# Kernel optimization log

Hardware: AMD Instinct MI355X
Metric: run time of the kernel (lower is better)

The kernel has to match this reference:

```python
import jax, jax.numpy as jnp
import numpy as np

MAX_DEG = 10
MIN_DEG = 0
N_FEAT = 128
NB_FILTER = 128
BATCH = 128
DEG_COUNT = 30000                      # atoms per degree bucket (static)
N_ATOMS = (MAX_DEG + 1) * DEG_COUNT    # 330000, atoms sorted by degree (deg0 first)
NB_AFFINE = 3 * MAX_DEG + (2 - MIN_DEG)  # 32
EPS = 1e-5


def setup_inputs() -> dict:
    key = jax.random.key(0)
    ks = jax.random.split(key, 16)
    atoms = jax.random.normal(ks[0], (N_ATOMS, N_FEAT), dtype=jnp.float32)
    membership = jax.random.randint(ks[1], (N_ATOMS,), 0, BATCH)
    # deg_slice[d] = [start, count] for degree d (atoms sorted by degree)
    deg_slice = jnp.stack([jnp.arange(MAX_DEG + 1) * DEG_COUNT,
                           jnp.full((MAX_DEG + 1,), DEG_COUNT)], axis=1)
    inp = {"atoms": atoms, "deg_slice": deg_slice, "membership": membership}
    for d in range(1, MAX_DEG + 1):
        inp[f"adj{d}"] = jax.random.randint(ks[1 + d], (DEG_COUNT, d), 0, N_ATOMS)
    glorot = (2.0 / (N_FEAT + NB_FILTER)) ** 0.5
    inp["W"] = jax.random.normal(ks[12], (NB_AFFINE, N_FEAT, NB_FILTER), dtype=jnp.float32) * glorot
    inp["b"] = jnp.zeros((NB_AFFINE, NB_FILTER), dtype=jnp.float32)
    inp["gamma"] = jnp.ones((NB_FILTER,), dtype=jnp.float32)
    inp["beta"] = jnp.zeros((NB_FILTER,), dtype=jnp.float32)
    return inp


def _self_slice(atoms, deg):
    return jax.lax.dynamic_slice_in_dim(atoms, deg * DEG_COUNT, DEG_COUNT, axis=0)


def _norm(x, gamma, beta):
    m = jnp.mean(x, axis=-1, keepdims=True)
    std = jnp.sqrt(jnp.var(x, axis=-1, keepdims=True) + EPS)
    return gamma * ((x - m) / (std + EPS)) + beta


def _forward(atoms, W, b, gamma, beta, membership, adjs):
    # W consumption order matches the TF iterator: for deg=1..max_deg -> (rel, self),
    # then deg0 self at index 2*MAX_DEG, then gather affines deg1..max_deg, deg0 last.
    rel_outs = [None] * (MAX_DEG + 1)
    gather_outs = [None] * (MAX_DEG + 1)
    for d in range(1, MAX_DEG + 1):
        neigh = jnp.sum(atoms[adjs[d - 1]], axis=1)          # (COUNT, F) gather+sum
        self_a = _self_slice(atoms, d)                        # (COUNT, F)
        i_rel, i_self = 2 * (d - 1), 2 * d - 1
        rel_outs[d] = (neigh @ W[i_rel] + b[i_rel]) + (self_a @ W[i_self] + b[i_self])
        i_g = 2 * MAX_DEG + d
        gather_outs[d] = self_a @ W[i_g] + b[i_g]
    self0 = _self_slice(atoms, 0)
    rel_outs[0] = self0 @ W[2 * MAX_DEG] + b[2 * MAX_DEG]
    gather_outs[0] = self0 @ W[NB_AFFINE - 1] + b[NB_AFFINE - 1]

    activated = jnp.concatenate(rel_outs, axis=0)             # (N_ATOMS, NB_FILTER)
    gathered = jnp.concatenate(gather_outs, axis=0)           # (N_ATOMS, NB_FILTER)
    # graph_gather: per-molecule sum (dynamic_partition + reduce_sum)
    atom_gather = jax.ops.segment_sum(gathered, membership, num_segments=BATCH)

    xn = _norm(activated, gamma, beta)                        # per-row "BN" as in source
    yn = _norm(atom_gather, gamma, beta)
    # gather_node: per-molecule max of normalized atom features
    g = jax.ops.segment_max(xn, membership, num_segments=BATCH)
    return xn, yn, g


def reference(atoms, deg_slice, membership, adj1, adj2, adj3, adj4, adj5,
              adj6, adj7, adj8, adj9, adj10, W, b, gamma, beta):
    adjs = (adj1, adj2, adj3, adj4, adj5, adj6, adj7, adj8, adj9, adj10)
    return _forward(atoms, W, b, gamma, beta, membership, adjs)
```

## Files before the change

### kernel.cpp

```cpp
#include <hip/hip_runtime.h>
#include <stdint.h>

#define MAX_DEG   10
#define DEG_COUNT 30000
#define N_ATOMS   330000
#define NF        128
#define BATCH     128
#define SORT_BLOCKS 256

typedef __attribute__((ext_vector_type(8))) short bf16x8;
typedef __attribute__((ext_vector_type(4))) float f32x4;

__device__ __forceinline__ float bf2f(unsigned short h) {
  union { unsigned u; float f; } v; v.u = ((unsigned)h) << 16; return v.f;
}
__device__ __forceinline__ unsigned short f2bf(float f) {
  union { float f; unsigned u; } v; v.f = f;
  unsigned u = v.u;
  unsigned r = (u + 0x7fffu + ((u >> 16) & 1u)) >> 16;
  return (unsigned short)r;
}

struct AdjPtrs { const int* p[10]; };

#define NEG_INF_BITS 0xFF800000

__global__ __launch_bounds__(256) void k_cast(const float4* __restrict__ src,
                                              ushort4* __restrict__ dst) {
  size_t i = (size_t)blockIdx.x * 256 + threadIdx.x;
  float4 v = src[i];
  ushort4 o;
  o.x = f2bf(v.x); o.y = f2bf(v.y); o.z = f2bf(v.z); o.w = f2bf(v.w);
  dst[i] = o;
}

__global__ __launch_bounds__(256) void k_build_b(const float* __restrict__ W,
                                                 unsigned short* __restrict__ BcatT) {
  int idx = blockIdx.x * 256 + threadIdx.x;
  if (idx >= 11 * 256 * 256) return;
  int d = idx >> 16;
  int rem = idx & 65535;
  int n = rem >> 8;
  int k = rem & 255;
  float v = 0.f;
  if (k < 128) {
    if (n < 128 && d >= 1) v = W[(2 * (d - 1)) * 16384 + k * 128 + n];
  } else {
    int ks = k - 128;
    if (n < 128) { int wi = (d >= 1) ? (2 * d - 1) : 20; v = W[wi * 16384 + ks * 128 + n]; }
    else         { int wi = (d >= 1) ? (20 + d)   : 31; v = W[wi * 16384 + ks * 128 + (n - 128)]; }
  }
  BcatT[idx] = f2bf(v);
}

__global__ __launch_bounds__(256) void k_build_bias(const float* __restrict__ b,
                                                    float* __restrict__ biascat) {
  int idx = blockIdx.x * 256 + threadIdx.x;
  if (idx >= 11 * 256) return;
  int d = idx >> 8, n = idx & 255;
  float f;
  if (n < 128) {
    if (d >= 1) f = b[(2 * (d - 1)) * 128 + n] + b[(2 * d - 1) * 128 + n];
    else        f = b[20 * 128 + n];
  } else {
    int j = n - 128;
    f = (d >= 1) ? b[(20 + d) * 128 + j] : b[31 * 128 + j];
  }
  biascat[idx] = f;
}

template<int D>
__device__ __forceinline__ void nsum_body2(const unsigned* __restrict__ atomsU,
                                           const int* __restrict__ a,
                                           int lane,
                                           unsigned* __restrict__ out) {
  int myIdx = (lane < 2 * D) ? a[lane] : 0;
  unsigned xs[2 * D];
#pragma unroll
  for (int j = 0; j < 2 * D; ++j) {
    int nbr = __shfl(myIdx, j, 64);
    xs[j] = atomsU[(size_t)nbr * 64 + lane];
  }
  float s0a = 0.f, s1a = 0.f, s0b = 0.f, s1b = 0.f;
#pragma unroll
  for (int j = 0; j < D; ++j) {
    s0a += bf2f((unsigned short)(xs[j] & 0xffff));
    s1a += bf2f((unsigned short)(xs[j] >> 16));
  }
#pragma unroll
  for (int j = D; j < 2 * D; ++j) {
    s0b += bf2f((unsigned short)(xs[j] & 0xffff));
    s1b += bf2f((unsigned short)(xs[j] >> 16));
  }
  out[lane]      = (unsigned)f2bf(s0a) | ((unsigned)f2bf(s1a) << 16);
  out[64 + lane] = (unsigned)f2bf(s0b) | ((unsigned)f2bf(s1b) << 16);
}

__global__ __launch_bounds__(256) void k_nsum(const unsigned* __restrict__ atomsU,
                                              AdjPtrs adj,
                                              unsigned* __restrict__ nsumU) {
  int wave = threadIdx.x >> 6;
  int lane = threadIdx.x & 63;
  int row0 = blockIdx.x * 8 + wave * 2;
  int d = row0 / DEG_COUNT;
  unsigned* out = nsumU + (size_t)row0 * 64;
  if (d == 0) { out[lane] = 0u; out[64 + lane] = 0u; return; }
  int r = row0 - d * DEG_COUNT;
  const int* a = adj.p[d - 1] + (size_t)r * d;
  switch (d) {
    case 1:  nsum_body2<1>(atomsU, a, lane, out); break;
    case 2:  nsum_body2<2>(atomsU, a, lane, out); break;
    case 3:  nsum_body2<3>(atomsU, a, lane, out); break;
    case 4:  nsum_body2<4>(atomsU, a, lane, out); break;
    case 5:  nsum_body2<5>(atomsU, a, lane, out); break;
    case 6:  nsum_body2<6>(atomsU, a, lane, out); break;
    case 7:  nsum_body2<7>(atomsU, a, lane, out); break;
    case 8:  nsum_body2<8>(atomsU, a, lane, out); break;
    case 9:  nsum_body2<9>(atomsU, a, lane, out); break;
    default: nsum_body2<10>(atomsU, a, lane, out); break;
  }
}

__global__ __launch_bounds__(512, 2) void k_gemm(
    const unsigned short* __restrict__ atomsBf,
    const unsigned short* __restrict__ nsum,
    const unsigned short* __restrict__ BcatT,
    const float* __restrict__ biascat,
    const float* __restrict__ gamma,
    const float* __restrict__ beta,
    float* __restrict__ out0,
    unsigned short* __restrict__ gath)
{
  const int d = blockIdx.y;
  const int rowTile = blockIdx.x;
  const int tid = threadIdx.x;
  const int lane = tid & 63;
  const int wave = tid >> 6;
  const int m16 = lane & 15;
  const int g = lane >> 4;

  __shared__ unsigned short Bs[256 * 256];

  const unsigned short* Bd = BcatT + d * 65536;

#pragma unroll
  for (int it = 0; it < 16; ++it) {
    int flat = it * 512 + tid;
    int row = flat >> 5;
    int c = flat & 31;
    uint4 v = *(const uint4*)(Bd + row * 256 + c * 8);
    int kb = (c * 16) ^ ((row & 7) << 4);
    *(uint4*)((char*)Bs + row * 512 + kb) = v;
  }

  const int rowBase0 = rowTile * 256 + wave * 32;
  bf16x8 af0[8], af1[8];
  {
    int rbL = rowBase0 + m16; if (rbL > DEG_COUNT - 1) rbL = DEG_COUNT - 1;
    size_t gr = (size_t)d * DEG_COUNT + rbL;
#pragma unroll
    for (int ks = 0; ks < 4; ++ks)
      af0[ks] = *(const bf16x8*)(nsum + gr * 128 + ks * 32 + g * 8);
#pragma unroll
    for (int ks = 4; ks < 8; ++ks)
      af0[ks] = *(const bf16x8*)(atomsBf + gr * 128 + (ks - 4) * 32 + g * 8);
  }
  {
    int rbL = rowBase0 + 16 + m16; if (rbL > DEG_COUNT - 1) rbL = DEG_COUNT - 1;
    size_t gr = (size_t)d * DEG_COUNT + rbL;
#pragma unroll
    for (int ks = 0; ks < 4; ++ks)
      af1[ks] = *(const bf16x8*)(nsum + gr * 128 + ks * 32 + g * 8);
#pragma unroll
    for (int ks = 4; ks < 8; ++ks)
      af1[ks] = *(const bf16x8*)(atomsBf + gr * 128 + (ks - 4) * 32 + g * 8);
  }

  __syncthreads();

  const int ldsMask = (m16 & 7) << 4;

  f32x4 acc0[16], acc1[16];
#pragma unroll
  for (int ct = 0; ct < 16; ++ct) {
    acc0[ct] = (f32x4){0.f, 0.f, 0.f, 0.f};
    acc1[ct] = (f32x4){0.f, 0.f, 0.f, 0.f};
  }

#pragma unroll
  for (int ct = 0; ct < 16; ++ct) {
    const char* bbase = (const char*)Bs + (ct * 16 + m16) * 512;
    bf16x8 bf[8];
#pragma unroll
    for (int ks = 0; ks < 8; ++ks)
      bf[ks] = *(const bf16x8*)(bbase + ((ks * 64 + g * 16) ^ ldsMask));
#pragma unroll
    for (int ks = 0; ks < 8; ++ks) {
      acc0[ct] = __builtin_amdgcn_mfma_f32_16x16x32_bf16(af0[ks], bf[ks], acc0[ct], 0, 0, 0);
      acc1[ct] = __builtin_amdgcn_mfma_f32_16x16x32_bf16(af1[ks], bf[ks], acc1[ct], 0, 0, 0);
    }
  }

  float bias_[16], gam[8], bet[8];
#pragma unroll
  for (int ct = 0; ct < 16; ++ct) bias_[ct] = biascat[d * 256 + ct * 16 + m16];
#pragma unroll
  for (int ct = 0; ct < 8; ++ct) {
    gam[ct] = gamma[ct * 16 + m16];
    bet[ct] = beta[ct * 16 + m16];
  }

#pragma unroll
  for (int sub = 0; sub < 2; ++sub) {
    const int rowBase = rowBase0 + sub * 16;
    f32x4* acc = (sub == 0) ? acc0 : acc1;

#pragma unroll
    for (int ct = 0; ct < 16; ++ct)
#pragma unroll
      for (int r = 0; r < 4; ++r) acc[ct][r] += bias_[ct];

    float s[4], qq[4];
#pragma unroll
    for (int r = 0; r < 4; ++r) {
      s[r] = 0.f; qq[r] = 0.f;
#pragma unroll
      for (int ct = 0; ct < 8; ++ct) {
        float v = acc[ct][r];
        s[r] += v; qq[r] += v * v;
      }
    }
#pragma unroll
    for (int off = 8; off >= 1; off >>= 1) {
#pragma unroll
      for (int r = 0; r < 4; ++r) {
        s[r]  += __shfl_xor(s[r],  off, 64);
        qq[r] += __shfl_xor(qq[r], off, 64);
      }
    }

#pragma unroll
    for (int r = 0; r < 4; ++r) {
      int rb = rowBase + g * 4 + r;
      float mean = s[r] * (1.0f / 128.0f);
      float var  = qq[r] * (1.0f / 128.0f) - mean * mean;
      float inv  = 1.0f / (sqrtf(var + 1e-5f) + 1e-5f);
      if (rb < DEG_COUNT) {
        size_t grow = (size_t)d * DEG_COUNT + rb;
#pragma unroll
        for (int ct = 0; ct < 8; ++ct)
          out0[grow * 128 + ct * 16 + m16] = gam[ct] * ((acc[ct][r] - mean) * inv) + bet[ct];
#pragma unroll
        for (int ct = 8; ct < 16; ++ct)
          gath[grow * 128 + (ct - 8) * 16 + m16] = f2bf(acc[ct][r]);
      }
    }
  }
}

__global__ __launch_bounds__(256) void k_hist2(const int* __restrict__ membership,
                                               int* __restrict__ blockHist) {
  __shared__ int bins[BATCH];
  int tid = threadIdx.x;
  if (tid < BATCH) bins[tid] = 0;
  __syncthreads();
  const int chunk = (N_ATOMS + SORT_BLOCKS - 1) / SORT_BLOCKS;
  int lo = blockIdx.x * chunk, hi = min(lo + chunk, N_ATOMS);
  for (int i = lo + tid; i < hi; i += 256)
    atomicAdd(&bins[membership[i]], 1);
  __syncthreads();
  if (tid < BATCH) blockHist[blockIdx.x * BATCH + tid] = bins[tid];
}

__global__ __launch_bounds__(128) void k_scan2(const int* __restrict__ blockHist,
                                               int* __restrict__ off,
                                               int* __restrict__ base,
                                               int* __restrict__ hist) {
  int m = threadIdx.x;
  int tot = 0;
  for (int b = 0; b < SORT_BLOCKS; ++b) tot += blockHist[b * BATCH + m];
  hist[m] = tot;
  __shared__ int t[BATCH];
  t[m] = tot;
  __syncthreads();
  int acc = 0;
  for (int i = 0; i < m; ++i) acc += t[i];
  base[m] = acc;
  int run = acc;
  for (int b = 0; b < SORT_BLOCKS; ++b) {
    off[b * BATCH + m] = run;
    run += blockHist[b * BATCH + m];
  }
}

__global__ __launch_bounds__(256) void k_scatter2(const int* __restrict__ membership,
                                                  const int* __restrict__ off,
                                                  int* __restrict__ perm) {
  __shared__ int bins[BATCH];
  int tid = threadIdx.x;
  if (tid < BATCH) bins[tid] = off[blockIdx.x * BATCH + tid];
  __syncthreads();
  const int chunk = (N_ATOMS + SORT_BLOCKS - 1) / SORT_BLOCKS;
  int lo = blockIdx.x * chunk, hi = min(lo + chunk, N_ATOMS);
  for (int i = lo + tid; i < hi; i += 256) {
    int m = membership[i];
    int pos = atomicAdd(&bins[m], 1);
    perm[pos] = i;
  }
}

__global__ __launch_bounds__(512) void k_reduce(
    const float2* __restrict__ xnV,
    const unsigned* __restrict__ gathU,
    const int* __restrict__ perm,
    const int* __restrict__ base,
    const int* __restrict__ hist,
    float2* __restrict__ psum4,
    float2* __restrict__ pmax4)
{
  const int m = blockIdx.x >> 2;
  const int s = blockIdx.x & 3;
  const int b0 = base[m], cnt = hist[m];
  const int lo = b0 + (cnt * s) / 4;
  const int hi = b0 + (cnt * (s + 1)) / 4;
  const int wave = threadIdx.x >> 6, lane = threadIdx.x & 63;

  const float NEG_INF = __int_as_float((int)NEG_INF_BITS);
  float mx0 = NEG_INF, mx1 = NEG_INF, s0 = 0.f, s1 = 0.f;

#pragma unroll 4
  for (int i = lo + wave; i < hi; i += 8) {
    int r = perm[i];
    float2 x = xnV[(size_t)r * 64 + lane];
    unsigned gg = gathU[(size_t)r * 64 + lane];
    mx0 = fmaxf(mx0, x.x);
    mx1 = fmaxf(mx1, x.y);
    s0 += bf2f((unsigned short)(gg & 0xffff));
    s1 += bf2f((unsigned short)(gg >> 16));
  }

  __shared__ float2 sumT[8][64];
  __shared__ float2 maxT[8][64];
  sumT[wave][lane] = make_float2(s0, s1);
  maxT[wave][lane] = make_float2(mx0, mx1);
  __syncthreads();

  if (threadIdx.x < 64) {
    int l = threadIdx.x;
    float2 ss = sumT[0][l];
    float2 mm = maxT[0][l];
#pragma unroll
    for (int w = 1; w < 8; ++w) {
      float2 a = sumT[w][l]; ss.x += a.x; ss.y += a.y;
      float2 b = maxT[w][l]; mm.x = fmaxf(mm.x, b.x); mm.y = fmaxf(mm.y, b.y);
    }
    psum4[(s * 128 + m) * 64 + l] = ss;
    pmax4[(s * 128 + m) * 64 + l] = mm;
  }
}

__global__ __launch_bounds__(128) void k_final(
    const float* __restrict__ psum4,
    const float* __restrict__ pmax4,
    const float* __restrict__ gamma,
    const float* __restrict__ beta,
    float* __restrict__ out1,
    float* __restrict__ out2)
{
  int m = blockIdx.x;
  int j = threadIdx.x;
  float s = 0.f, g = __int_as_float((int)NEG_INF_BITS);
#pragma unroll
  for (int sl = 0; sl < 4; ++sl) {
    s += psum4[(sl * 128 + m) * 128 + j];
    g = fmaxf(g, pmax4[(sl * 128 + m) * 128 + j]);
  }
  out2[m * 128 + j] = g;

  float ws_ = s, wq = s * s;
#pragma unroll
  for (int off = 32; off >= 1; off >>= 1) {
    ws_ += __shfl_xor(ws_, off, 64);
    wq  += __shfl_xor(wq, off, 64);
  }
  __shared__ float red[4];
  int wave = j >> 6, lane = j & 63;
  if (lane == 0) { red[wave * 2] = ws_; red[wave * 2 + 1] = wq; }
  __syncthreads();
  float S = red[0] + red[2], Q = red[1] + red[3];
  float mean = S * (1.f / 128.f);
  float var = Q * (1.f / 128.f) - mean * mean;
  float inv = 1.f / (sqrtf(var + 1e-5f) + 1e-5f);
  float yn = gamma[j] * ((s - mean) * inv) + beta[j];
  out1[m * 128 + j] = yn;
}

extern "C" void kernel_launch(void* const* d_in, const int* in_sizes, int n_in,
                              void* d_out, int out_size, void* d_ws, size_t ws_size,
                              hipStream_t stream) {
  const float* atoms = (const float*)d_in[0];
  const int* membership = (const int*)d_in[2];
  AdjPtrs adj;
  for (int i = 0; i < 10; ++i) adj.p[i] = (const int*)d_in[3 + i];
  const float* W     = (const float*)d_in[13];
  const float* b     = (const float*)d_in[14];
  const float* gamma = (const float*)d_in[15];
  const float* beta  = (const float*)d_in[16];

  char* ws = (char*)d_ws;
  size_t off = 0;
  unsigned short* atomsBf = (unsigned short*)(ws + off); off += (size_t)N_ATOMS * 128 * 2;
  unsigned short* nsum    = (unsigned short*)(ws + off); off += (size_t)N_ATOMS * 128 * 2;
  unsigned short* gath    = (unsigned short*)(ws + off); off += (size_t)N_ATOMS * 128 * 2;
  unsigned short* BcatT   = (unsigned short*)(ws + off); off += (size_t)11 * 256 * 256 * 2;
  float* biascat          = (float*)(ws + off);          off += (size_t)11 * 256 * 4;

  char* scr = (char*)atomsBf;
  int* perm      = (int*)(scr);
  int* hist      = (int*)(scr + 2 * 1024 * 1024);
  int* base_     = (int*)(scr + 2 * 1024 * 1024 + 1024);
  int* blockHist = (int*)(scr + 2 * 1024 * 1024 + 4096);
  int* offTab    = (int*)(scr + 2 * 1024 * 1024 + 4096 + SORT_BLOCKS * BATCH * 4);
  float* psum4   = (float*)(scr + 3 * 1024 * 1024);
  float* pmax4   = (float*)(scr + 3 * 1024 * 1024 + 256 * 1024);

  float* out0 = (float*)d_out;
  float* out1 = out0 + (size_t)N_ATOMS * 128;
  float* out2 = out1 + 16384;

  hipLaunchKernelGGL(k_cast, dim3(N_ATOMS * 128 / 4 / 256), dim3(256), 0, stream,
                     (const float4*)atoms, (ushort4*)atomsBf);
  hipLaunchKernelGGL(k_build_b, dim3((11 * 256 * 256 + 255) / 256), dim3(256), 0, stream, W, BcatT);
  hipLaunchKernelGGL(k_build_bias, dim3((11 * 256 + 255) / 256), dim3(256), 0, stream, b, biascat);
  hipLaunchKernelGGL(k_nsum, dim3(N_ATOMS / 8), dim3(256), 0, stream,
                     (const unsigned*)atomsBf, adj, (unsigned*)nsum);
  hipLaunchKernelGGL(k_gemm, dim3(118, 11), dim3(512), 0, stream,
                     atomsBf, nsum, BcatT, biascat, gamma, beta, out0, gath);
  hipLaunchKernelGGL(k_hist2, dim3(SORT_BLOCKS), dim3(256), 0, stream, membership, blockHist);
  hipLaunchKernelGGL(k_scan2, dim3(1), dim3(128), 0, stream, blockHist, offTab, base_, hist);
  hipLaunchKernelGGL(k_scatter2, dim3(SORT_BLOCKS), dim3(256), 0, stream, membership, offTab, perm);
  hipLaunchKernelGGL(k_reduce, dim3(512), dim3(512), 0, stream,
                     (const float2*)out0, (const unsigned*)gath, perm, base_, hist,
                     (float2*)psum4, (float2*)pmax4);
  hipLaunchKernelGGL(k_final, dim3(128), dim3(128), 0, stream,
                     psum4, pmax4, gamma, beta, out1, out2);
}
```

Before: 561.2 us.

## Fuse neighbor gather-sum into GEMM kernel via shared-memory staging

Removes the standalone neighbor-sum kernel and computes the neighbor sums inside the GEMM kernel. Each block gathers its 256 rows' neighbor features into swizzled LDS, reads them back as MFMA A fragments, then reuses the same LDS for the weight tile. This avoids writing and re-reading the bf16 nsum buffer in global memory and saves a launch. In exchange, the gather latency is serialized inside each GEMM block, with only 2 blocks per CU, and the weight load is delayed until after the gather.

```diff
diff --git a/kernel.cpp b/kernel.cpp
--- a/kernel.cpp
+++ b/kernel.cpp
@@ -70,60 +70,62 @@
 }
 
 template<int D>
-__device__ __forceinline__ void nsum_body2(const unsigned* __restrict__ atomsU,
-                                           const int* __restrict__ a,
-                                           int lane,
-                                           unsigned* __restrict__ out) {
-  int myIdx = (lane < 2 * D) ? a[lane] : 0;
-  unsigned xs[2 * D];
-#pragma unroll
-  for (int j = 0; j < 2 * D; ++j) {
-    int nbr = __shfl(myIdx, j, 64);
-    xs[j] = atomsU[(size_t)nbr * 64 + lane];
-  }
-  float s0a = 0.f, s1a = 0.f, s0b = 0.f, s1b = 0.f;
-#pragma unroll
-  for (int j = 0; j < D; ++j) {
-    s0a += bf2f((unsigned short)(xs[j] & 0xffff));
-    s1a += bf2f((unsigned short)(xs[j] >> 16));
-  }
-#pragma unroll
-  for (int j = D; j < 2 * D; ++j) {
-    s0b += bf2f((unsigned short)(xs[j] & 0xffff));
-    s1b += bf2f((unsigned short)(xs[j] >> 16));
-  }
-  out[lane]      = (unsigned)f2bf(s0a) | ((unsigned)f2bf(s1a) << 16);
-  out[64 + lane] = (unsigned)f2bf(s0b) | ((unsigned)f2bf(s1b) << 16);
-}
-
-__global__ __launch_bounds__(256) void k_nsum(const unsigned* __restrict__ atomsU,
-                                              AdjPtrs adj,
-                                              unsigned* __restrict__ nsumU) {
-  int wave = threadIdx.x >> 6;
-  int lane = threadIdx.x & 63;
-  int row0 = blockIdx.x * 8 + wave * 2;
-  int d = row0 / DEG_COUNT;
-  unsigned* out = nsumU + (size_t)row0 * 64;
-  if (d == 0) { out[lane] = 0u; out[64 + lane] = 0u; return; }
-  int r = row0 - d * DEG_COUNT;
-  const int* a = adj.p[d - 1] + (size_t)r * d;
-  switch (d) {
-    case 1:  nsum_body2<1>(atomsU, a, lane, out); break;
-    case 2:  nsum_body2<2>(atomsU, a, lane, out); break;
-    case 3:  nsum_body2<3>(atomsU, a, lane, out); break;
-    case 4:  nsum_body2<4>(atomsU, a, lane, out); break;
-    case 5:  nsum_body2<5>(atomsU, a, lane, out); break;
-    case 6:  nsum_body2<6>(atomsU, a, lane, out); break;
-    case 7:  nsum_body2<7>(atomsU, a, lane, out); break;
-    case 8:  nsum_body2<8>(atomsU, a, lane, out); break;
-    case 9:  nsum_body2<9>(atomsU, a, lane, out); break;
-    default: nsum_body2<10>(atomsU, a, lane, out); break;
+__device__ __forceinline__ void nsum_phase0(const unsigned* __restrict__ atomsU,
+                                            const int* __restrict__ abase,
+                                            unsigned* __restrict__ NS,
+                                            int rowTile, int wave, int lane) {
+  for (int it = 0; it < 16; ++it) {
+    int iloc = wave * 32 + it * 2;
+    int r0 = rowTile * 256 + iloc;
+    int sw0 = lane ^ ((iloc & 7) << 2);
+    int sw1 = lane ^ (((iloc + 1) & 7) << 2);
+    if (r0 < DEG_COUNT - 1) {
+      const int* a = abase + (size_t)r0 * D;
+      int myIdx = (lane < 2 * D) ? a[lane] : 0;
+      unsigned xs[2 * D];
+#pragma unroll
+      for (int j = 0; j < 2 * D; ++j) {
+        int nbr = __shfl(myIdx, j, 64);
+        xs[j] = atomsU[(size_t)nbr * 64 + lane];
+      }
+      float s0a = 0.f, s1a = 0.f, s0b = 0.f, s1b = 0.f;
+#pragma unroll
+      for (int j = 0; j < D; ++j) {
+        s0a += bf2f((unsigned short)(xs[j] & 0xffff));
+        s1a += bf2f((unsigned short)(xs[j] >> 16));
+      }
+#pragma unroll
+      for (int j = D; j < 2 * D; ++j) {
+        s0b += bf2f((unsigned short)(xs[j] & 0xffff));
+        s1b += bf2f((unsigned short)(xs[j] >> 16));
+      }
+      NS[(size_t)iloc * 64 + sw0]       = (unsigned)f2bf(s0a) | ((unsigned)f2bf(s1a) << 16);
+      NS[(size_t)(iloc + 1) * 64 + sw1] = (unsigned)f2bf(s0b) | ((unsigned)f2bf(s1b) << 16);
+    } else {
+      const int* a = abase + (size_t)(DEG_COUNT - 1) * D;
+      int myIdx = (lane < D) ? a[lane] : 0;
+      unsigned xs[D];
+#pragma unroll
+      for (int j = 0; j < D; ++j) {
+        int nbr = __shfl(myIdx, j, 64);
+        xs[j] = atomsU[(size_t)nbr * 64 + lane];
+      }
+      float s0 = 0.f, s1 = 0.f;
+#pragma unroll
+      for (int j = 0; j < D; ++j) {
+        s0 += bf2f((unsigned short)(xs[j] & 0xffff));
+        s1 += bf2f((unsigned short)(xs[j] >> 16));
+      }
+      unsigned p = (unsigned)f2bf(s0) | ((unsigned)f2bf(s1) << 16);
+      NS[(size_t)iloc * 64 + sw0] = p;
+      NS[(size_t)(iloc + 1) * 64 + sw1] = p;
+    }
   }
 }
 
 __global__ __launch_bounds__(512, 2) void k_gemm(
     const unsigned short* __restrict__ atomsBf,
-    const unsigned short* __restrict__ nsum,
+    AdjPtrs adj,
     const unsigned short* __restrict__ BcatT,
     const float* __restrict__ biascat,
     const float* __restrict__ gamma,
@@ -140,8 +142,58 @@
   const int g = lane >> 4;
 
   __shared__ unsigned short Bs[256 * 256];
+  unsigned* NS = (unsigned*)Bs;
 
   const unsigned short* Bd = BcatT + d * 65536;
+  const unsigned* atomsU = (const unsigned*)atomsBf;
+
+  const int rowBase0 = rowTile * 256 + wave * 32;
+  bf16x8 af0[8], af1[8];
+  {
+    int rbL = rowBase0 + m16; if (rbL > DEG_COUNT - 1) rbL = DEG_COUNT - 1;
+    size_t gr = (size_t)d * DEG_COUNT + rbL;
+#pragma unroll
+    for (int ks = 4; ks < 8; ++ks)
+      af0[ks] = *(const bf16x8*)(atomsBf + gr * 128 + (ks - 4) * 32 + g * 8);
+  }
+  {
+    int rbL = rowBase0 + 16 + m16; if (rbL > DEG_COUNT - 1) rbL = DEG_COUNT - 1;
+    size_t gr = (size_t)d * DEG_COUNT + rbL;
+#pragma unroll
+    for (int ks = 4; ks < 8; ++ks)
+      af1[ks] = *(const bf16x8*)(atomsBf + gr * 128 + (ks - 4) * 32 + g * 8);
+  }
+
+  if (d > 0) {
+    const int* abase = adj.p[d - 1];
+    switch (d) {
+      case 1:  nsum_phase0<1>(atomsU, abase, NS, rowTile, wave, lane); break;
+      case 2:  nsum_phase0<2>(atomsU, abase, NS, rowTile, wave, lane); break;
+      case 3:  nsum_phase0<3>(atomsU, abase, NS, rowTile, wave, lane); break;
+      case 4:  nsum_phase0<4>(atomsU, abase, NS, rowTile, wave, lane); break;
+      case 5:  nsum_phase0<5>(atomsU, abase, NS, rowTile, wave, lane); break;
+      case 6:  nsum_phase0<6>(atomsU, abase, NS, rowTile, wave, lane); break;
+      case 7:  nsum_phase0<7>(atomsU, abase, NS, rowTile, wave, lane); break;
+      case 8:  nsum_phase0<8>(atomsU, abase, NS, rowTile, wave, lane); break;
+      case 9:  nsum_phase0<9>(atomsU, abase, NS, rowTile, wave, lane); break;
+      default: nsum_phase0<10>(atomsU, abase, NS, rowTile, wave, lane); break;
+    }
+    __syncthreads();
+    const char* nsb = (const char*)NS;
+    const int rowb0 = (wave * 32 + m16) * 256;
+    const int rowb1 = (wave * 32 + 16 + m16) * 256;
+    const int sw = (m16 & 7) << 4;
+#pragma unroll
+    for (int ks = 0; ks < 4; ++ks) {
+      af0[ks] = *(const bf16x8*)(nsb + ((rowb0 + ks * 64 + g * 16) ^ sw));
+      af1[ks] = *(const bf16x8*)(nsb + ((rowb1 + ks * 64 + g * 16) ^ sw));
+    }
+    __syncthreads();
+  } else {
+    bf16x8 z = {0, 0, 0, 0, 0, 0, 0, 0};
+#pragma unroll
+    for (int ks = 0; ks < 4; ++ks) { af0[ks] = z; af1[ks] = z; }
+  }
 
 #pragma unroll
   for (int it = 0; it < 16; ++it) {
@@ -151,29 +203,6 @@
     uint4 v = *(const uint4*)(Bd + row * 256 + c * 8);
     int kb = (c * 16) ^ ((row & 7) << 4);
     *(uint4*)((char*)Bs + row * 512 + kb) = v;
-  }
-
-  const int rowBase0 = rowTile * 256 + wave * 32;
-  bf16x8 af0[8], af1[8];
-  {
-    int rbL = rowBase0 + m16; if (rbL > DEG_COUNT - 1) rbL = DEG_COUNT - 1;
-    size_t gr = (size_t)d * DEG_COUNT + rbL;
-#pragma unroll
-    for (int ks = 0; ks < 4; ++ks)
-      af0[ks] = *(const bf16x8*)(nsum + gr * 128 + ks * 32 + g * 8);
-#pragma unroll
-    for (int ks = 4; ks < 8; ++ks)
-      af0[ks] = *(const bf16x8*)(atomsBf + gr * 128 + (ks - 4) * 32 + g * 8);
-  }
-  {
-    int rbL = rowBase0 + 16 + m16; if (rbL > DEG_COUNT - 1) rbL = DEG_COUNT - 1;
-    size_t gr = (size_t)d * DEG_COUNT + rbL;
-#pragma unroll
-    for (int ks = 0; ks < 4; ++ks)
-      af1[ks] = *(const bf16x8*)(nsum + gr * 128 + ks * 32 + g * 8);
-#pragma unroll
-    for (int ks = 4; ks < 8; ++ks)
-      af1[ks] = *(const bf16x8*)(atomsBf + gr * 128 + (ks - 4) * 32 + g * 8);
   }
 
   __syncthreads();
@@ -414,6 +443,7 @@
   unsigned short* gath    = (unsigned short*)(ws + off); off += (size_t)N_ATOMS * 128 * 2;
   unsigned short* BcatT   = (unsigned short*)(ws + off); off += (size_t)11 * 256 * 256 * 2;
   float* biascat          = (float*)(ws + off);          off += (size_t)11 * 256 * 4;
+  (void)nsum;
 
   char* scr = (char*)atomsBf;
   int* perm      = (int*)(scr);
@@ -432,10 +462,8 @@
                      (const float4*)atoms, (ushort4*)atomsBf);
   hipLaunchKernelGGL(k_build_b, dim3((11 * 256 * 256 + 255) / 256), dim3(256), 0, stream, W, BcatT);
   hipLaunchKernelGGL(k_build_bias, dim3((11 * 256 + 255) / 256), dim3(256), 0, stream, b, biascat);
-  hipLaunchKernelGGL(k_nsum, dim3(N_ATOMS / 8), dim3(256), 0, stream,
-                     (const unsigned*)atomsBf, adj, (unsigned*)nsum);
   hipLaunchKernelGGL(k_gemm, dim3(118, 11), dim3(512), 0, stream,
-                     atomsBf, nsum, BcatT, biascat, gamma, beta, out0, gath);
+                     atomsBf, adj, BcatT, biascat, gamma, beta, out0, gath);
   hipLaunchKernelGGL(k_hist2, dim3(SORT_BLOCKS), dim3(256), 0, stream, membership, blockHist);
   hipLaunchKernelGGL(k_scan2, dim3(1), dim3(128), 0, stream, blockHist, offTab, base_, hist);
   hipLaunchKernelGGL(k_scatter2, dim3(SORT_BLOCKS), dim3(256), 0, stream, membership, offTab, perm);
```

New measurement: 554.2 us. About the same (-1.2%).
